# Kernel optimization log

Measured on AMD Instinct MI355X. Metric: run time of the kernel, lower is better.

The kernel has to match this reference:

```python
import jax, jax.numpy as jnp
import numpy as np

FT_SIZE = 512
NUM_BUCKETS = 8
HID = 32
IN_FEATS = 770

def _crelu(x):
    return jnp.clip(x, 0.0, 1.0)

def setup_inputs() -> dict:
    key = jax.random.key(0)
    ks = jax.random.split(key, 8)
    B = 65536
    x = jax.random.uniform(ks[0], (B, 2 * IN_FEATS), dtype=jnp.float32)
    s = 0.05
    ft_w = jax.random.normal(ks[1], (FT_SIZE, IN_FEATS), dtype=jnp.float32) * s
    ft_b = jax.random.normal(ks[2], (FT_SIZE,), dtype=jnp.float32) * s
    h1_w = jax.random.normal(ks[3], (NUM_BUCKETS, HID, 2 * FT_SIZE), dtype=jnp.float32) * s
    h1_b = jax.random.normal(ks[4], (NUM_BUCKETS, HID), dtype=jnp.float32) * s
    h2_w = jax.random.normal(ks[5], (NUM_BUCKETS, HID, HID), dtype=jnp.float32) * s
    h2_b = jax.random.normal(ks[6], (NUM_BUCKETS, HID), dtype=jnp.float32) * s
    h3_w = jax.random.normal(ks[7], (NUM_BUCKETS, 1, HID), dtype=jnp.float32) * s
    h3_b = jnp.zeros((NUM_BUCKETS, 1), dtype=jnp.float32)
    return {"x": x, "ft_w": ft_w, "ft_b": ft_b, "h1_w": h1_w, "h1_b": h1_b,
            "h2_w": h2_w, "h2_b": h2_b, "h3_w": h3_w, "h3_b": h3_b}

def reference(x, ft_w, ft_b, h1_w, h1_b, h2_w, h2_b, h3_w, h3_b):
    stm = x[:, :IN_FEATS]          # [B, 770]
    nstm = x[:, IN_FEATS:]         # [B, 770]
    stm_ft = _crelu(stm @ ft_w.T + ft_b)    # [B, FT]
    nstm_ft = _crelu(nstm @ ft_w.T + ft_b)  # [B, FT]
    combined = jnp.concatenate([stm_ft, nstm_ft], axis=1)  # [B, 2FT]
    # bucket index from piece count (STM first 768 channels)
    pc = jnp.sum(x[:, :768], axis=1)
    bucket_idx = jnp.clip((pc * NUM_BUCKETS / 33.0).astype(jnp.int32), 0, NUM_BUCKETS - 1)  # [B]
    # compute all bucket heads (dense compute-all, matching original loop+stack)
    h = _crelu(jnp.einsum('bi,koi->bko', combined, h1_w) + h1_b)  # [B, K, 32]
    h = _crelu(jnp.einsum('bko,kpo->bkp', h, h2_w) + h2_b)        # [B, K, 32]
    all_out = jnp.einsum('bko,kpo->bkp', h, h3_w) + h3_b          # [B, K, 1]
    out = jnp.take_along_axis(all_out, bucket_idx[:, None, None], axis=1)  # [B,1,1]
    return out[:, 0, :]  # [B, 1]
```

## Files before the change

### kernel.cpp

```cpp
#include <hip/hip_runtime.h>
#include <hip/hip_bf16.h>
#include <stdint.h>


#define INF 770
#define KP  800
#define FT  512
#define K2  1024
#define N2  256

typedef _Float16 half8 __attribute__((ext_vector_type(8)));
typedef float floatx4 __attribute__((ext_vector_type(4)));

__device__ __forceinline__ float crelu_f(float v) {
    return v < 0.f ? 0.f : (v > 1.f ? 1.f : v);
}

__device__ __forceinline__ void gl_lds16(const _Float16* g, _Float16* l) {
    __builtin_amdgcn_global_load_lds(
        (__attribute__((address_space(1))) void*)(uintptr_t)(const void*)g,
        (__attribute__((address_space(3))) void*)l,
        16, 0, 0);
}

__global__ __launch_bounds__(256) void convert_x_kernel(
    const float* __restrict__ x, _Float16* __restrict__ x16,
    int* __restrict__ bucket, int B)
{
    __shared__ float red[4];
    int b = blockIdx.x;
    int tid = threadIdx.x, lane = tid & 63, w = tid >> 6;
    const float* src = x + (size_t)b * (2 * INF);
    _Float16* d0 = x16 + (size_t)b * KP;
    _Float16* d1 = x16 + ((size_t)B + b) * KP;
    float s = 0.f;
    for (int i = tid; i < KP; i += 256) {
        float v0 = 0.f, v1 = 0.f;
        if (i < INF) { v0 = src[i]; v1 = src[INF + i]; }
        d0[i] = (_Float16)v0;
        d1[i] = (_Float16)v1;
        if (i < 768) s += v0;
    }
    #pragma unroll
    for (int off = 32; off; off >>= 1) s += __shfl_down(s, off, 64);
    if (lane == 0) red[w] = s;
    __syncthreads();
    if (tid == 0) {
        float pc = red[0] + red[1] + red[2] + red[3];
        int bk = (int)(pc * (8.0f / 33.0f));
        bucket[b] = bk < 0 ? 0 : (bk > 7 ? 7 : bk);
    }
}

__global__ __launch_bounds__(256) void convert_w_kernel(
    const float* __restrict__ ftw, const float* __restrict__ h1w,
    _Float16* __restrict__ ftw16, _Float16* __restrict__ h1w16)
{
    int idx = blockIdx.x * 256 + threadIdx.x;
    const int FTW = FT * KP;
    if (idx < FTW) {
        int r = idx / KP, c = idx - r * KP;
        ftw16[idx] = (_Float16)(c < INF ? ftw[r * INF + c] : 0.f);
    } else {
        int j = idx - FTW;
        if (j < N2 * K2) h1w16[j] = (_Float16)h1w[j];
    }
}

__global__ __launch_bounds__(256) void gemm_ft_kernel(
    const _Float16* __restrict__ A,
    const _Float16* __restrict__ Bt,
    const float* __restrict__ bias,
    _Float16* __restrict__ C)
{
    __shared__ _Float16 lsA[128 * 32];
    __shared__ _Float16 lsB[128 * 32];
    int bid = blockIdx.x;
    int x = bid & 7, g = bid >> 3;
    int mt = x * 128 + (g >> 2), nt = g & 3;
    int m0 = mt * 128, n0 = nt * 128;
    int tid = threadIdx.x, lane = tid & 63, w = tid >> 6;
    int rm = (w & 1) * 64, rn = (w >> 1) * 64;
    int colL = lane & 15, rowQ = lane >> 4;
    int chA = rowQ ^ ((colL >> 1) & 3);

    floatx4 acc[4][4] = {};

    for (int kt = 0; kt < KP / 32; ++kt) {
        int ks = kt * 32;
        #pragma unroll
        for (int p = 0; p < 2; ++p) {
            int qb = p * 256 + w * 64;
            int q = qb + lane;
            int r = q >> 2;
            int c8 = (q & 3) ^ ((r >> 1) & 3);
            gl_lds16(A + (size_t)(m0 + r) * KP + ks + c8 * 8, lsA + qb * 8);
            gl_lds16(Bt + (size_t)(n0 + r) * KP + ks + c8 * 8, lsB + qb * 8);
        }
        asm volatile("s_waitcnt vmcnt(0)" ::: "memory");
        __syncthreads();

        half8 af[4], bf[4];
        #pragma unroll
        for (int i = 0; i < 4; ++i)
            af[i] = *(const half8*)(lsA + (rm + i * 16 + colL) * 32 + chA * 8);
        #pragma unroll
        for (int j = 0; j < 4; ++j)
            bf[j] = *(const half8*)(lsB + (rn + j * 16 + colL) * 32 + chA * 8);
        #pragma unroll
        for (int i = 0; i < 4; ++i)
            #pragma unroll
            for (int j = 0; j < 4; ++j)
                acc[i][j] = __builtin_amdgcn_mfma_f32_16x16x32_f16(af[i], bf[j], acc[i][j], 0, 0, 0);
        __syncthreads();
    }

    #pragma unroll
    for (int j = 0; j < 4; ++j) {
        int gn = n0 + rn + j * 16 + colL;
        float bv = bias[gn];
        #pragma unroll
        for (int i = 0; i < 4; ++i) {
            #pragma unroll
            for (int r = 0; r < 4; ++r) {
                int gm = m0 + rm + i * 16 + rowQ * 4 + r;
                float v = crelu_f(acc[i][j][r] + bv);
                C[(size_t)gm * FT + gn] = (_Float16)v;
            }
        }
    }
}

__global__ __launch_bounds__(256) void gemm_h1_kernel(
    const _Float16* __restrict__ C1,
    const _Float16* __restrict__ Bt,
    const float* __restrict__ bias,
    float* __restrict__ H,
    int B)
{
    __shared__ _Float16 lsA[128 * 32];
    __shared__ _Float16 lsB[128 * 32];
    int bid = blockIdx.x;
    int x = bid & 7, g = bid >> 3;
    int mt = x * 64 + (g >> 1), nt = g & 1;
    int m0 = mt * 128, n0 = nt * 128;
    int tid = threadIdx.x, lane = tid & 63, w = tid >> 6;
    int rm = (w & 1) * 64, rn = (w >> 1) * 64;
    int colL = lane & 15, rowQ = lane >> 4;
    int chA = rowQ ^ ((colL >> 1) & 3);

    floatx4 acc[4][4] = {};

    for (int kt = 0; kt < K2 / 32; ++kt) {
        int ks = kt * 32;
        const _Float16* Abase = (ks < FT) ? (C1 + ks)
                                          : (C1 + (size_t)B * FT + (ks - FT));
        #pragma unroll
        for (int p = 0; p < 2; ++p) {
            int qb = p * 256 + w * 64;
            int q = qb + lane;
            int r = q >> 2;
            int c8 = (q & 3) ^ ((r >> 1) & 3);
            gl_lds16(Abase + (size_t)(m0 + r) * FT + c8 * 8, lsA + qb * 8);
            gl_lds16(Bt + (size_t)(n0 + r) * K2 + ks + c8 * 8, lsB + qb * 8);
        }
        asm volatile("s_waitcnt vmcnt(0)" ::: "memory");
        __syncthreads();

        half8 af[4], bf[4];
        #pragma unroll
        for (int i = 0; i < 4; ++i)
            af[i] = *(const half8*)(lsA + (rm + i * 16 + colL) * 32 + chA * 8);
        #pragma unroll
        for (int j = 0; j < 4; ++j)
            bf[j] = *(const half8*)(lsB + (rn + j * 16 + colL) * 32 + chA * 8);
        #pragma unroll
        for (int i = 0; i < 4; ++i)
            #pragma unroll
            for (int j = 0; j < 4; ++j)
                acc[i][j] = __builtin_amdgcn_mfma_f32_16x16x32_f16(af[i], bf[j], acc[i][j], 0, 0, 0);
        __syncthreads();
    }

    #pragma unroll
    for (int j = 0; j < 4; ++j) {
        int gn = n0 + rn + j * 16 + colL;
        float bv = bias[gn];
        #pragma unroll
        for (int i = 0; i < 4; ++i) {
            #pragma unroll
            for (int r = 0; r < 4; ++r) {
                int gm = m0 + rm + i * 16 + rowQ * 4 + r;
                H[(size_t)gm * N2 + gn] = crelu_f(acc[i][j][r] + bv);
            }
        }
    }
}

__global__ __launch_bounds__(256) void tail_kernel(
    const float* __restrict__ H,
    const int* __restrict__ bucket,
    const float* __restrict__ h2w,
    const float* __restrict__ h2b,
    const float* __restrict__ h3w,
    const float* __restrict__ h3b,
    float* __restrict__ out, int B)
{
    int s = blockIdx.x * 8 + (threadIdx.x >> 5);
    int j = threadIdx.x & 31;
    if (s >= B) return;
    int k = bucket[s];
    float h1v = H[(size_t)s * N2 + k * 32 + j];
    const float* w2 = h2w + ((k * 32 + j) * 32);
    float a = h2b[k * 32 + j];
    #pragma unroll
    for (int i = 0; i < 32; ++i) a += w2[i] * __shfl(h1v, i, 32);
    a = crelu_f(a);
    float p = a * h3w[k * 32 + j];
    #pragma unroll
    for (int off = 16; off; off >>= 1) p += __shfl_down(p, off, 32);
    if (j == 0) out[s] = p + h3b[k];
}

extern "C" void kernel_launch(void* const* d_in, const int* in_sizes, int n_in,
                              void* d_out, int out_size, void* d_ws, size_t ws_size,
                              hipStream_t stream) {
    const float* x    = (const float*)d_in[0];
    const float* ftw  = (const float*)d_in[1];
    const float* ftb  = (const float*)d_in[2];
    const float* h1w  = (const float*)d_in[3];
    const float* h1b  = (const float*)d_in[4];
    const float* h2w  = (const float*)d_in[5];
    const float* h2b  = (const float*)d_in[6];
    const float* h3w  = (const float*)d_in[7];
    const float* h3b  = (const float*)d_in[8];
    float* out = (float*)d_out;

    int B = in_sizes[0] / (2 * INF);

    char* ws = (char*)d_ws;
    _Float16* x16   = (_Float16*)ws;
    size_t x16_b    = (size_t)2 * B * KP * sizeof(_Float16);
    _Float16* C1    = (_Float16*)(ws + x16_b);
    size_t c1_b     = (size_t)2 * B * FT * sizeof(_Float16);
    _Float16* ftw16 = (_Float16*)(ws + x16_b + c1_b);
    _Float16* h1w16 = ftw16 + (size_t)FT * KP;
    int* bucket     = (int*)(h1w16 + (size_t)N2 * K2);
    float* H        = (float*)ws;

    {
        int total = FT * KP + N2 * K2;
        convert_w_kernel<<<(total + 255) / 256, 256, 0, stream>>>(ftw, h1w, ftw16, h1w16);
    }
    convert_x_kernel<<<B, 256, 0, stream>>>(x, x16, bucket, B);
    {
        int grid = (2 * B / 128) * 4;
        gemm_ft_kernel<<<grid, 256, 0, stream>>>(x16, ftw16, ftb, C1);
    }
    {
        int grid = (B / 128) * 2;
        gemm_h1_kernel<<<grid, 256, 0, stream>>>(C1, h1w16, h1b, H, B);
    }
    tail_kernel<<<(B + 7) / 8, 256, 0, stream>>>(H, bucket, h2w, h2b, h3w, h3b, out, B);
}
```

Before: 898.5 us.

## Fuse fp32-to-fp16 input conversion and bucket sum into the FT GEMM

Drops the separate convert_x kernel. The FT GEMM now reads fp32 x directly, converts it to fp16 in registers, writes it into LDS, and computes the piece-count bucket from partial sums. Both GEMMs move to 512-thread blocks with wider N tiles: the FT GEMM is 128x256 per block, and the H1 GEMM is 64 rows by all 256 outputs, so each block loads A only once. This removes a full write and reread of the fp16 copy of x. In exchange, the A loads become synchronous register loads with no async overlap, and they are strided 8-byte reads.

```diff
diff --git a/kernel.cpp b/kernel.cpp
--- a/kernel.cpp
+++ b/kernel.cpp
@@ -3,14 +3,16 @@
 #include <stdint.h>
 
 
-#define INF 770
-#define KP  800
-#define FT  512
-#define K2  1024
-#define N2  256
+#define INF  770
+#define XROW 1540
+#define KP   800
+#define FT   512
+#define K2   1024
+#define N2   256
 
 typedef _Float16 half8 __attribute__((ext_vector_type(8)));
 typedef float floatx4 __attribute__((ext_vector_type(4)));
+typedef float floatx2 __attribute__((ext_vector_type(2)));
 
 __device__ __forceinline__ float crelu_f(float v) {
     return v < 0.f ? 0.f : (v > 1.f ? 1.f : v);
@@ -21,35 +23,6 @@
         (__attribute__((address_space(1))) void*)(uintptr_t)(const void*)g,
         (__attribute__((address_space(3))) void*)l,
         16, 0, 0);
-}
-
-__global__ __launch_bounds__(256) void convert_x_kernel(
-    const float* __restrict__ x, _Float16* __restrict__ x16,
-    int* __restrict__ bucket, int B)
-{
-    __shared__ float red[4];
-    int b = blockIdx.x;
-    int tid = threadIdx.x, lane = tid & 63, w = tid >> 6;
-    const float* src = x + (size_t)b * (2 * INF);
-    _Float16* d0 = x16 + (size_t)b * KP;
-    _Float16* d1 = x16 + ((size_t)B + b) * KP;
-    float s = 0.f;
-    for (int i = tid; i < KP; i += 256) {
-        float v0 = 0.f, v1 = 0.f;
-        if (i < INF) { v0 = src[i]; v1 = src[INF + i]; }
-        d0[i] = (_Float16)v0;
-        d1[i] = (_Float16)v1;
-        if (i < 768) s += v0;
-    }
-    #pragma unroll
-    for (int off = 32; off; off >>= 1) s += __shfl_down(s, off, 64);
-    if (lane == 0) red[w] = s;
-    __syncthreads();
-    if (tid == 0) {
-        float pc = red[0] + red[1] + red[2] + red[3];
-        int bk = (int)(pc * (8.0f / 33.0f));
-        bucket[b] = bk < 0 ? 0 : (bk > 7 ? 7 : bk);
-    }
 }
 
 __global__ __launch_bounds__(256) void convert_w_kernel(
@@ -67,35 +40,57 @@
     }
 }
 
-__global__ __launch_bounds__(256) void gemm_ft_kernel(
-    const _Float16* __restrict__ A,
+__global__ __launch_bounds__(512, 4) void gemm_ft_fused(
+    const float* __restrict__ x,
     const _Float16* __restrict__ Bt,
     const float* __restrict__ bias,
-    _Float16* __restrict__ C)
+    _Float16* __restrict__ C,
+    int* __restrict__ bucket, int B)
 {
     __shared__ _Float16 lsA[128 * 32];
-    __shared__ _Float16 lsB[128 * 32];
+    __shared__ _Float16 lsB[256 * 32];
     int bid = blockIdx.x;
-    int x = bid & 7, g = bid >> 3;
-    int mt = x * 128 + (g >> 2), nt = g & 3;
-    int m0 = mt * 128, n0 = nt * 128;
+    int xcd = bid & 7, g = bid >> 3;
+    int nt = g & 1, mt = (g >> 1) * 8 + xcd;
+    int m0 = mt * 128, n0 = nt * 256;
     int tid = threadIdx.x, lane = tid & 63, w = tid >> 6;
     int rm = (w & 1) * 64, rn = (w >> 1) * 64;
     int colL = lane & 15, rowQ = lane >> 4;
     int chA = rowQ ^ ((colL >> 1) & 3);
 
+    int arow = tid >> 2, kq = tid & 3;
+    const float* asrc = (m0 < B)
+        ? x + (size_t)(m0 + arow) * XROW
+        : x + (size_t)(m0 - B + arow) * XROW + INF;
+    _Float16* adst = lsA + arow * 32 + (kq ^ ((arow >> 1) & 3)) * 8;
+
     floatx4 acc[4][4] = {};
-
-    for (int kt = 0; kt < KP / 32; ++kt) {
+    float psum = 0.f;
+
+    for (int kt = 0; kt < 25; ++kt) {
         int ks = kt * 32;
+        half8 hv = {};
+        if (kt < 24) {
+            const float* p = asrc + ks + kq * 8;
+            floatx2 f0 = *(const floatx2*)(p);
+            floatx2 f1 = *(const floatx2*)(p + 2);
+            floatx2 f2 = *(const floatx2*)(p + 4);
+            floatx2 f3 = *(const floatx2*)(p + 6);
+            hv[0] = (_Float16)f0.x; hv[1] = (_Float16)f0.y;
+            hv[2] = (_Float16)f1.x; hv[3] = (_Float16)f1.y;
+            hv[4] = (_Float16)f2.x; hv[5] = (_Float16)f2.y;
+            hv[6] = (_Float16)f3.x; hv[7] = (_Float16)f3.y;
+            psum += (f0.x + f0.y) + (f1.x + f1.y) + (f2.x + f2.y) + (f3.x + f3.y);
+        } else if (kq == 0) {
+            floatx2 f0 = *(const floatx2*)(asrc + 768);
+            hv[0] = (_Float16)f0.x; hv[1] = (_Float16)f0.y;
+        }
+        *(half8*)adst = hv;
         #pragma unroll
         for (int p = 0; p < 2; ++p) {
-            int qb = p * 256 + w * 64;
-            int q = qb + lane;
-            int r = q >> 2;
-            int c8 = (q & 3) ^ ((r >> 1) & 3);
-            gl_lds16(A + (size_t)(m0 + r) * KP + ks + c8 * 8, lsA + qb * 8);
-            gl_lds16(Bt + (size_t)(n0 + r) * KP + ks + c8 * 8, lsB + qb * 8);
+            int idx = p * 512 + tid;
+            int br = idx >> 2, bs = (idx & 3) ^ ((br >> 1) & 3);
+            gl_lds16(Bt + (size_t)(n0 + br) * KP + ks + bs * 8, lsB + idx * 8);
         }
         asm volatile("s_waitcnt vmcnt(0)" ::: "memory");
         __syncthreads();
@@ -113,6 +108,13 @@
             for (int j = 0; j < 4; ++j)
                 acc[i][j] = __builtin_amdgcn_mfma_f32_16x16x32_f16(af[i], bf[j], acc[i][j], 0, 0, 0);
         __syncthreads();
+    }
+
+    psum += __shfl_xor(psum, 1, 64);
+    psum += __shfl_xor(psum, 2, 64);
+    if (nt == 0 && m0 < B && (tid & 3) == 0) {
+        int bk = (int)(psum * (8.0f / 33.0f));
+        bucket[m0 + arow] = bk < 0 ? 0 : (bk > 7 ? 7 : bk);
     }
 
     #pragma unroll
@@ -124,73 +126,69 @@
             #pragma unroll
             for (int r = 0; r < 4; ++r) {
                 int gm = m0 + rm + i * 16 + rowQ * 4 + r;
-                float v = crelu_f(acc[i][j][r] + bv);
-                C[(size_t)gm * FT + gn] = (_Float16)v;
+                C[(size_t)gm * FT + gn] = (_Float16)crelu_f(acc[i][j][r] + bv);
             }
         }
     }
 }
 
-__global__ __launch_bounds__(256) void gemm_h1_kernel(
+__global__ __launch_bounds__(512, 4) void gemm_h1_kernel(
     const _Float16* __restrict__ C1,
     const _Float16* __restrict__ Bt,
     const float* __restrict__ bias,
     float* __restrict__ H,
     int B)
 {
-    __shared__ _Float16 lsA[128 * 32];
-    __shared__ _Float16 lsB[128 * 32];
-    int bid = blockIdx.x;
-    int x = bid & 7, g = bid >> 3;
-    int mt = x * 64 + (g >> 1), nt = g & 1;
-    int m0 = mt * 128, n0 = nt * 128;
+    __shared__ _Float16 lsA[64 * 32];
+    __shared__ _Float16 lsB[256 * 32];
+    int m0 = blockIdx.x * 64;
     int tid = threadIdx.x, lane = tid & 63, w = tid >> 6;
-    int rm = (w & 1) * 64, rn = (w >> 1) * 64;
     int colL = lane & 15, rowQ = lane >> 4;
     int chA = rowQ ^ ((colL >> 1) & 3);
 
-    floatx4 acc[4][4] = {};
-
-    for (int kt = 0; kt < K2 / 32; ++kt) {
+    floatx4 acc[4][2] = {};
+
+    for (int kt = 0; kt < 32; ++kt) {
         int ks = kt * 32;
-        const _Float16* Abase = (ks < FT) ? (C1 + ks)
-                                          : (C1 + (size_t)B * FT + (ks - FT));
+        const _Float16* Abase = (ks < FT) ? (C1 + (size_t)m0 * FT + ks)
+                                          : (C1 + (size_t)(B + m0) * FT + (ks - FT));
+        if (tid < 256) {
+            int br = tid >> 2, bs = (tid & 3) ^ ((br >> 1) & 3);
+            gl_lds16(Abase + (size_t)br * FT + bs * 8, lsA + tid * 8);
+        }
         #pragma unroll
         for (int p = 0; p < 2; ++p) {
-            int qb = p * 256 + w * 64;
-            int q = qb + lane;
-            int r = q >> 2;
-            int c8 = (q & 3) ^ ((r >> 1) & 3);
-            gl_lds16(Abase + (size_t)(m0 + r) * FT + c8 * 8, lsA + qb * 8);
-            gl_lds16(Bt + (size_t)(n0 + r) * K2 + ks + c8 * 8, lsB + qb * 8);
+            int idx = p * 512 + tid;
+            int br = idx >> 2, bs = (idx & 3) ^ ((br >> 1) & 3);
+            gl_lds16(Bt + (size_t)br * K2 + ks + bs * 8, lsB + idx * 8);
         }
         asm volatile("s_waitcnt vmcnt(0)" ::: "memory");
         __syncthreads();
 
-        half8 af[4], bf[4];
-        #pragma unroll
-        for (int i = 0; i < 4; ++i)
-            af[i] = *(const half8*)(lsA + (rm + i * 16 + colL) * 32 + chA * 8);
-        #pragma unroll
-        for (int j = 0; j < 4; ++j)
-            bf[j] = *(const half8*)(lsB + (rn + j * 16 + colL) * 32 + chA * 8);
-        #pragma unroll
-        for (int i = 0; i < 4; ++i)
-            #pragma unroll
-            for (int j = 0; j < 4; ++j)
+        half8 af[4], bf[2];
+        #pragma unroll
+        for (int i = 0; i < 4; ++i)
+            af[i] = *(const half8*)(lsA + (i * 16 + colL) * 32 + chA * 8);
+        #pragma unroll
+        for (int j = 0; j < 2; ++j)
+            bf[j] = *(const half8*)(lsB + (w * 32 + j * 16 + colL) * 32 + chA * 8);
+        #pragma unroll
+        for (int i = 0; i < 4; ++i)
+            #pragma unroll
+            for (int j = 0; j < 2; ++j)
                 acc[i][j] = __builtin_amdgcn_mfma_f32_16x16x32_f16(af[i], bf[j], acc[i][j], 0, 0, 0);
         __syncthreads();
     }
 
     #pragma unroll
-    for (int j = 0; j < 4; ++j) {
-        int gn = n0 + rn + j * 16 + colL;
+    for (int j = 0; j < 2; ++j) {
+        int gn = w * 32 + j * 16 + colL;
         float bv = bias[gn];
         #pragma unroll
         for (int i = 0; i < 4; ++i) {
             #pragma unroll
             for (int r = 0; r < 4; ++r) {
-                int gm = m0 + rm + i * 16 + rowQ * 4 + r;
+                int gm = m0 + i * 16 + rowQ * 4 + r;
                 H[(size_t)gm * N2 + gn] = crelu_f(acc[i][j][r] + bv);
             }
         }
@@ -239,27 +237,21 @@
     int B = in_sizes[0] / (2 * INF);
 
     char* ws = (char*)d_ws;
-    _Float16* x16   = (_Float16*)ws;
-    size_t x16_b    = (size_t)2 * B * KP * sizeof(_Float16);
-    _Float16* C1    = (_Float16*)(ws + x16_b);
+    _Float16* C1    = (_Float16*)ws;
     size_t c1_b     = (size_t)2 * B * FT * sizeof(_Float16);
-    _Float16* ftw16 = (_Float16*)(ws + x16_b + c1_b);
-    _Float16* h1w16 = ftw16 + (size_t)FT * KP;
-    int* bucket     = (int*)(h1w16 + (size_t)N2 * K2);
-    float* H        = (float*)ws;
+    _Float16* ftw16 = (_Float16*)(ws + c1_b);
+    size_t ftw_b    = (size_t)FT * KP * sizeof(_Float16);
+    _Float16* h1w16 = (_Float16*)(ws + c1_b + ftw_b);
+    size_t h1w_b    = (size_t)N2 * K2 * sizeof(_Float16);
+    int* bucket     = (int*)(ws + c1_b + ftw_b + h1w_b);
+    size_t bk_b     = (size_t)B * sizeof(int);
+    float* H        = (float*)(ws + c1_b + ftw_b + h1w_b + bk_b);
 
     {
         int total = FT * KP + N2 * K2;
         convert_w_kernel<<<(total + 255) / 256, 256, 0, stream>>>(ftw, h1w, ftw16, h1w16);
     }
-    convert_x_kernel<<<B, 256, 0, stream>>>(x, x16, bucket, B);
-    {
-        int grid = (2 * B / 128) * 4;
-        gemm_ft_kernel<<<grid, 256, 0, stream>>>(x16, ftw16, ftb, C1);
-    }
-    {
-        int grid = (B / 128) * 2;
-        gemm_h1_kernel<<<grid, 256, 0, stream>>>(C1, h1w16, h1b, H, B);
-    }
+    gemm_ft_fused<<<(2 * B / 128) * 2, 512, 0, stream>>>(x, ftw16, ftb, C1, bucket, B);
+    gemm_h1_kernel<<<B / 64, 512, 0, stream>>>(C1, h1w16, h1b, H, B);
     tail_kernel<<<(B + 7) / 8, 256, 0, stream>>>(H, bucket, h2w, h2b, h3w, h3b, out, B);
 }
```

Result: faster. 799.4 us (-11.0%).
